# Optimization experiments

Hardware: AMD Instinct MI355X
Metric: run time of the kernel (lower is better)

Reference implementation:

```python
import jax, jax.numpy as jnp
import numpy as np

ETA = 0.15
LAM = 0.05
K = 6


def setup_inputs() -> dict:
    key = jax.random.key(0)
    ks = jax.random.split(key, 9)
    Bsz, L, d, hidden = 32, 8192, 64, 256
    scale = lambda fan_in: 1.0 / np.sqrt(fan_in)
    return {
        "A": jax.random.normal(ks[0], (Bsz, L, d), jnp.float32),
        "B": jax.random.normal(ks[1], (Bsz, L, d), jnp.float32),
        "q": jax.random.normal(ks[2], (Bsz, L, d), jnp.float32),
        "W1": jax.random.normal(ks[3], (2 * d, hidden), jnp.float32) * scale(2 * d),
        "b1": jax.random.normal(ks[4], (hidden,), jnp.float32) * 0.01,
        "W2": jax.random.normal(ks[5], (hidden, d), jnp.float32) * scale(hidden),
        "b2": jax.random.normal(ks[6], (d,), jnp.float32) * 0.01,
        "Wq": jax.random.normal(ks[7], (d, d), jnp.float32) * scale(d),
        "bq": jax.random.normal(ks[8], (d,), jnp.float32) * 0.01,
    }


def _smooth1d(x):
    return x - LAM * (2.0 * x - jnp.roll(x, 1, axis=1) - jnp.roll(x, -1, axis=1))


def reference(A, B, q, W1, b1, W2, b2, Wq, bq):
    # mu_net: Linear -> ReLU -> Linear -> Softplus on concat([A,B])
    h = jnp.concatenate([A, B], axis=-1)  # [B, L, 2d]
    mu = jax.nn.softplus(jax.nn.relu(h @ W1 + b1) @ W2 + b2)  # [B, L, d]
    gate = jnp.tanh(q @ Wq + bq)
    mu = mu * (1.0 + 0.5 * gate)

    hA, hB = A, B
    for _ in range(K):
        step = ETA * (mu * (hA - hB))
        hA = _smooth1d(hA - step)
        hB = _smooth1d(hB + step)

    energy = 0.5 * jnp.sum(mu * jnp.square(hA - hB), axis=(1, 2))  # [B]
    return hA, hB, energy
```

## Files before the change

kernel.cpp:

```cpp
#include <hip/hip_runtime.h>
#include <hip/hip_bf16.h>
#include <hip/hip_fp16.h>

#define ETA 0.15f
#define LAM 0.05f

typedef unsigned int uint32;
typedef __attribute__((ext_vector_type(8))) short short8;
typedef __attribute__((ext_vector_type(4))) float floatx4;

static const int BSZ = 32, LL = 8192, DD = 64;
static const int RTOT = BSZ * LL;

static const size_t MU_BYTES = (size_t)RTOT * DD * 2;
static const size_t W1T_OFF  = MU_BYTES;
static const size_t W2T_OFF  = W1T_OFF + 256 * 128 * 2;
static const size_t WQT_OFF  = W2T_OFF + 64 * 256 * 2;

__device__ __forceinline__ unsigned short f2bf(float f) {
    uint32 u = __builtin_bit_cast(uint32, f);
    uint32 r = (u + 0x7FFFu + ((u >> 16) & 1u)) >> 16;
    return (unsigned short)r;
}

__device__ __forceinline__ float fast_softplus(float x) {
    return fmaxf(x, 0.f) + __logf(1.f + __expf(-fabsf(x)));
}
__device__ __forceinline__ float fast_tanh(float x) {
    float t = __expf(-2.f * fabsf(x));
    float r = (1.f - t) / (1.f + t);
    return copysignf(r, x);
}

__global__ void prep_kernel(const float* __restrict__ W1, const float* __restrict__ W2,
                            const float* __restrict__ Wq,
                            unsigned short* __restrict__ w1t, unsigned short* __restrict__ w2t,
                            unsigned short* __restrict__ wqt, float* __restrict__ energy) {
    int tid = blockIdx.x * blockDim.x + threadIdx.x;
    int nth = gridDim.x * blockDim.x;
    for (int i = tid; i < 256 * 128; i += nth) { int n = i >> 7, k = i & 127; w1t[i] = f2bf(W1[k * 256 + n]); }
    for (int i = tid; i < 64 * 256; i += nth) { int n = i >> 8, k = i & 255; w2t[i] = f2bf(W2[k * 64 + n]); }
    for (int i = tid; i < 64 * 64;  i += nth) { int n = i >> 6, k = i & 63;  wqt[i] = f2bf(Wq[k * 64 + n]); }
    if (tid < 32) energy[tid] = 0.f;
}

__global__ __launch_bounds__(256) void mlp_kernel(
    const float* __restrict__ A, const float* __restrict__ B, const float* __restrict__ Q,
    const float* __restrict__ b1, const float* __restrict__ b2, const float* __restrict__ bq,
    const unsigned short* __restrict__ w1t, const unsigned short* __restrict__ w2t,
    const unsigned short* __restrict__ wqt, _Float16* __restrict__ mu_out) {
    __shared__ char lds[61440];
    unsigned short* Xs = (unsigned short*)(lds);
    unsigned short* Zs = (unsigned short*)(lds + 17408);
    unsigned short* Qs = (unsigned short*)(lds + 17408 + 34816);

    const int tid = threadIdx.x;
    const int lane = tid & 63;
    const int w = tid >> 6;
    const int q4 = lane >> 4;
    const int l16 = lane & 15;
    const int rowbase = blockIdx.x * 64;

    uint32* Xu = (uint32*)Xs;
    for (int i = tid; i < 64 * 64; i += 256) {
        int r = i >> 6, j2 = i & 63;
        const float* src = (j2 < 32) ? (A + (size_t)(rowbase + r) * 64 + 2 * j2)
                                     : (B + (size_t)(rowbase + r) * 64 + 2 * (j2 - 32));
        float2 v = *(const float2*)src;
        Xu[r * 68 + j2] = (uint32)f2bf(v.x) | ((uint32)f2bf(v.y) << 16);
    }
    uint32* Qu = (uint32*)Qs;
    for (int i = tid; i < 64 * 32; i += 256) {
        int r = i >> 5, j2 = i & 31;
        float2 v = *(const float2*)(Q + (size_t)(rowbase + r) * 64 + 2 * j2);
        Qu[r * 36 + j2] = (uint32)f2bf(v.x) | ((uint32)f2bf(v.y) << 16);
    }
    __syncthreads();

    short8 ax[4][4];
#pragma unroll
    for (int m = 0; m < 4; m++)
#pragma unroll
        for (int kt = 0; kt < 4; kt++)
            ax[m][kt] = *(const short8*)&Xs[(m * 16 + l16) * 136 + kt * 32 + q4 * 8];

#pragma unroll
    for (int nt = 0; nt < 4; nt++) {
        const int ng = w * 4 + nt;
        short8 wf[4];
#pragma unroll
        for (int kt = 0; kt < 4; kt++)
            wf[kt] = *(const short8*)&w1t[(ng * 16 + l16) * 128 + kt * 32 + q4 * 8];
        floatx4 acc[4];
#pragma unroll
        for (int m = 0; m < 4; m++) acc[m] = (floatx4){0.f, 0.f, 0.f, 0.f};
#pragma unroll
        for (int kt = 0; kt < 4; kt++)
#pragma unroll
            for (int m = 0; m < 4; m++)
                acc[m] = __builtin_amdgcn_mfma_f32_16x16x32_bf16(ax[m][kt], wf[kt], acc[m], 0, 0, 0);
        const int col = ng * 16 + l16;
        const float b1v = b1[col];
#pragma unroll
        for (int m = 0; m < 4; m++)
#pragma unroll
            for (int r = 0; r < 4; r++) {
                float z = acc[m][r] + b1v;
                z = z > 0.f ? z : 0.f;
                Zs[(m * 16 + q4 * 4 + r) * 272 + col] = f2bf(z);
            }
    }
    short8 w2f[8], wqf[2];
#pragma unroll
    for (int kt = 0; kt < 8; kt++)
        w2f[kt] = *(const short8*)&w2t[(w * 16 + l16) * 256 + kt * 32 + q4 * 8];
#pragma unroll
    for (int kt = 0; kt < 2; kt++)
        wqf[kt] = *(const short8*)&wqt[(w * 16 + l16) * 64 + kt * 32 + q4 * 8];
    __syncthreads();

    floatx4 acc2[4], acc3[4];
#pragma unroll
    for (int m = 0; m < 4; m++) { acc2[m] = (floatx4){0.f,0.f,0.f,0.f}; acc3[m] = (floatx4){0.f,0.f,0.f,0.f}; }
#pragma unroll
    for (int m = 0; m < 4; m++)
#pragma unroll
        for (int kt = 0; kt < 8; kt++) {
            short8 az = *(const short8*)&Zs[(m * 16 + l16) * 272 + kt * 32 + q4 * 8];
            acc2[m] = __builtin_amdgcn_mfma_f32_16x16x32_bf16(az, w2f[kt], acc2[m], 0, 0, 0);
        }
#pragma unroll
    for (int m = 0; m < 4; m++)
#pragma unroll
        for (int kt = 0; kt < 2; kt++) {
            short8 aq = *(const short8*)&Qs[(m * 16 + l16) * 72 + kt * 32 + q4 * 8];
            acc3[m] = __builtin_amdgcn_mfma_f32_16x16x32_bf16(aq, wqf[kt], acc3[m], 0, 0, 0);
        }
    const int col = w * 16 + l16;
    const float b2v = b2[col], bqv = bq[col];
#pragma unroll
    for (int m = 0; m < 4; m++)
#pragma unroll
        for (int r = 0; r < 4; r++) {
            int row = m * 16 + q4 * 4 + r;
            float sp = fast_softplus(acc2[m][r] + b2v);
            float g = fast_tanh(acc3[m][r] + bqv);
            float mu = sp * (1.f + 0.5f * g);
            mu_out[(size_t)(rowbase + row) * 64 + col] = (_Float16)mu;
        }
}

__global__ __launch_bounds__(256) void iter_kernel(
    const float* __restrict__ A, const float* __restrict__ B, const _Float16* __restrict__ mu_ws,
    float* __restrict__ outA, float* __restrict__ outB, float* __restrict__ energy) {
    __shared__ float ex[2][4][4][64];
    __shared__ float esm[4];
    const int tid = threadIdx.x;
    const int col = tid & 63;
    const int g = tid >> 6;
    const int b = blockIdx.y;
    const int s = blockIdx.x * 64;
    const size_t bbase = (size_t)b * 8192;
    const int r0 = g * 19;

    float a[19], bv[19], me[19];
#pragma unroll
    for (int i = 0; i < 19; i++) {
        int gl = (s + r0 + i + 8192 - 6) & 8191;
        size_t idx = (bbase + gl) * 64 + col;
        a[i] = A[idx];
        bv[i] = B[idx];
        me[i] = ETA * (float)mu_ws[idx];
    }
    for (int it = 0; it < 6; it++) {
        float st[19];
#pragma unroll
        for (int i = 0; i < 19; i++) st[i] = me[i] * (a[i] - bv[i]);
        float* exb = &ex[it & 1][0][0][0];
        exb[0 * 256 + g * 64 + col] = a[0] - st[0];
        exb[1 * 256 + g * 64 + col] = a[18] - st[18];
        exb[2 * 256 + g * 64 + col] = bv[0] + st[0];
        exb[3 * 256 + g * 64 + col] = bv[18] + st[18];
        __syncthreads();
        float tAup = (g > 0) ? exb[1 * 256 + (g - 1) * 64 + col] : a[0] - st[0];
        float tAdn = (g < 3) ? exb[0 * 256 + (g + 1) * 64 + col] : a[18] - st[18];
        float tBup = (g > 0) ? exb[3 * 256 + (g - 1) * 64 + col] : bv[0] + st[0];
        float tBdn = (g < 3) ? exb[2 * 256 + (g + 1) * 64 + col] : bv[18] + st[18];
        float prev = tAup, cur = a[0] - st[0];
#pragma unroll
        for (int i = 0; i < 19; i++) {
            float nxt = (i < 18) ? (a[i + 1] - st[i + 1]) : tAdn;
            a[i] = cur - LAM * (2.f * cur - prev - nxt);
            prev = cur; cur = nxt;
        }
        prev = tBup; cur = bv[0] + st[0];
#pragma unroll
        for (int i = 0; i < 19; i++) {
            float nxt = (i < 18) ? (bv[i + 1] + st[i + 1]) : tBdn;
            bv[i] = cur - LAM * (2.f * cur - prev - nxt);
            prev = cur; cur = nxt;
        }
    }
    float e = 0.f;
#pragma unroll
    for (int i = 0; i < 19; i++) {
        int r = r0 + i;
        if (r >= 6 && r < 70) {
            float d = a[i] - bv[i];
            e += me[i] * d * d;
            size_t gidx = (bbase + s + (r - 6)) * 64 + col;
            outA[gidx] = a[i];
            outB[gidx] = bv[i];
        }
    }
    e *= 0.5f / ETA;
#pragma unroll
    for (int off = 32; off > 0; off >>= 1) e += __shfl_down(e, off, 64);
    if ((tid & 63) == 0) esm[g] = e;
    __syncthreads();
    if (tid == 0) atomicAdd(energy + b, esm[0] + esm[1] + esm[2] + esm[3]);
}

extern "C" void kernel_launch(void* const* d_in, const int* in_sizes, int n_in,
                              void* d_out, int out_size, void* d_ws, size_t ws_size,
                              hipStream_t stream) {
    const float* A  = (const float*)d_in[0];
    const float* B  = (const float*)d_in[1];
    const float* Q  = (const float*)d_in[2];
    const float* W1 = (const float*)d_in[3];
    const float* b1 = (const float*)d_in[4];
    const float* W2 = (const float*)d_in[5];
    const float* b2 = (const float*)d_in[6];
    const float* Wq = (const float*)d_in[7];
    const float* bq = (const float*)d_in[8];

    float* outA = (float*)d_out;
    float* outB = outA + (size_t)RTOT * 64;
    float* energy = outB + (size_t)RTOT * 64;

    char* ws = (char*)d_ws;
    _Float16* mu_ws = (_Float16*)ws;
    unsigned short* w1t = (unsigned short*)(ws + W1T_OFF);
    unsigned short* w2t = (unsigned short*)(ws + W2T_OFF);
    unsigned short* wqt = (unsigned short*)(ws + WQT_OFF);

    hipLaunchKernelGGL(prep_kernel, dim3(64), dim3(256), 0, stream,
                       W1, W2, Wq, w1t, w2t, wqt, energy);
    hipLaunchKernelGGL(mlp_kernel, dim3(RTOT / 64), dim3(256), 0, stream,
                       A, B, Q, b1, b2, bq, w1t, w2t, wqt, mu_ws);
    hipLaunchKernelGGL(iter_kernel, dim3(LL / 64, BSZ), dim3(256), 0, stream,
                       A, B, mu_ws, outA, outB, energy);
}
```

Before: 414.1 us.

## Vectorize iter kernel with float4 rows and shrink MLP LDS by aliasing buffers

The iteration kernel now gives each thread 4 adjacent columns as float4 and splits a 80-row window (halo 8) across 16 row groups of 5 rows, replacing 19 scalar rows per thread. This is meant to cut register pressure and use wider global and LDS accesses, at the cost of more halo recomputation per tile. The MLP kernel computes the gate GEMM first and then reuses the X region for Z, shrinking LDS from 60KB to 34KB so more blocks fit per CU. That reuse needs an extra barrier.

```diff
diff --git a/kernel.cpp b/kernel.cpp
--- a/kernel.cpp
+++ b/kernel.cpp
@@ -8,6 +8,7 @@
 typedef unsigned int uint32;
 typedef __attribute__((ext_vector_type(8))) short short8;
 typedef __attribute__((ext_vector_type(4))) float floatx4;
+typedef __attribute__((ext_vector_type(4))) _Float16 half4;
 
 static const int BSZ = 32, LL = 8192, DD = 64;
 static const int RTOT = BSZ * LL;
@@ -22,7 +23,6 @@
     uint32 r = (u + 0x7FFFu + ((u >> 16) & 1u)) >> 16;
     return (unsigned short)r;
 }
-
 __device__ __forceinline__ float fast_softplus(float x) {
     return fmaxf(x, 0.f) + __logf(1.f + __expf(-fabsf(x)));
 }
@@ -49,10 +49,10 @@
     const float* __restrict__ b1, const float* __restrict__ b2, const float* __restrict__ bq,
     const unsigned short* __restrict__ w1t, const unsigned short* __restrict__ w2t,
     const unsigned short* __restrict__ wqt, _Float16* __restrict__ mu_out) {
-    __shared__ char lds[61440];
+    __shared__ char lds[34816];
     unsigned short* Xs = (unsigned short*)(lds);
-    unsigned short* Zs = (unsigned short*)(lds + 17408);
-    unsigned short* Qs = (unsigned short*)(lds + 17408 + 34816);
+    unsigned short* Qs = (unsigned short*)(lds + 17408);
+    unsigned short* Zs = (unsigned short*)(lds);
 
     const int tid = threadIdx.x;
     const int lane = tid & 63;
@@ -77,12 +77,29 @@
     }
     __syncthreads();
 
+    floatx4 acc3[4];
+#pragma unroll
+    for (int m = 0; m < 4; m++) acc3[m] = (floatx4){0.f, 0.f, 0.f, 0.f};
+    {
+        short8 wqf[2];
+#pragma unroll
+        for (int kt = 0; kt < 2; kt++)
+            wqf[kt] = *(const short8*)&wqt[(w * 16 + l16) * 64 + kt * 32 + q4 * 8];
+#pragma unroll
+        for (int m = 0; m < 4; m++)
+#pragma unroll
+            for (int kt = 0; kt < 2; kt++) {
+                short8 aq = *(const short8*)&Qs[(m * 16 + l16) * 72 + kt * 32 + q4 * 8];
+                acc3[m] = __builtin_amdgcn_mfma_f32_16x16x32_bf16(aq, wqf[kt], acc3[m], 0, 0, 0);
+            }
+    }
     short8 ax[4][4];
 #pragma unroll
     for (int m = 0; m < 4; m++)
 #pragma unroll
         for (int kt = 0; kt < 4; kt++)
             ax[m][kt] = *(const short8*)&Xs[(m * 16 + l16) * 136 + kt * 32 + q4 * 8];
+    __syncthreads();
 
 #pragma unroll
     for (int nt = 0; nt < 4; nt++) {
@@ -110,31 +127,21 @@
                 Zs[(m * 16 + q4 * 4 + r) * 272 + col] = f2bf(z);
             }
     }
-    short8 w2f[8], wqf[2];
+    short8 w2f[8];
 #pragma unroll
     for (int kt = 0; kt < 8; kt++)
         w2f[kt] = *(const short8*)&w2t[(w * 16 + l16) * 256 + kt * 32 + q4 * 8];
-#pragma unroll
-    for (int kt = 0; kt < 2; kt++)
-        wqf[kt] = *(const short8*)&wqt[(w * 16 + l16) * 64 + kt * 32 + q4 * 8];
-    __syncthreads();
-
-    floatx4 acc2[4], acc3[4];
-#pragma unroll
-    for (int m = 0; m < 4; m++) { acc2[m] = (floatx4){0.f,0.f,0.f,0.f}; acc3[m] = (floatx4){0.f,0.f,0.f,0.f}; }
+    __syncthreads();
+
+    floatx4 acc2[4];
+#pragma unroll
+    for (int m = 0; m < 4; m++) acc2[m] = (floatx4){0.f, 0.f, 0.f, 0.f};
 #pragma unroll
     for (int m = 0; m < 4; m++)
 #pragma unroll
         for (int kt = 0; kt < 8; kt++) {
             short8 az = *(const short8*)&Zs[(m * 16 + l16) * 272 + kt * 32 + q4 * 8];
             acc2[m] = __builtin_amdgcn_mfma_f32_16x16x32_bf16(az, w2f[kt], acc2[m], 0, 0, 0);
-        }
-#pragma unroll
-    for (int m = 0; m < 4; m++)
-#pragma unroll
-        for (int kt = 0; kt < 2; kt++) {
-            short8 aq = *(const short8*)&Qs[(m * 16 + l16) * 72 + kt * 32 + q4 * 8];
-            acc3[m] = __builtin_amdgcn_mfma_f32_16x16x32_bf16(aq, wqf[kt], acc3[m], 0, 0, 0);
         }
     const int col = w * 16 + l16;
     const float b2v = b2[col], bqv = bq[col];
@@ -153,70 +160,75 @@
 __global__ __launch_bounds__(256) void iter_kernel(
     const float* __restrict__ A, const float* __restrict__ B, const _Float16* __restrict__ mu_ws,
     float* __restrict__ outA, float* __restrict__ outB, float* __restrict__ energy) {
-    __shared__ float ex[2][4][4][64];
+    __shared__ float ex[2][4][16][64];
     __shared__ float esm[4];
     const int tid = threadIdx.x;
-    const int col = tid & 63;
-    const int g = tid >> 6;
+    const int c4 = tid & 15;
+    const int g = tid >> 4;
     const int b = blockIdx.y;
     const int s = blockIdx.x * 64;
     const size_t bbase = (size_t)b * 8192;
-    const int r0 = g * 19;
-
-    float a[19], bv[19], me[19];
-#pragma unroll
-    for (int i = 0; i < 19; i++) {
-        int gl = (s + r0 + i + 8192 - 6) & 8191;
-        size_t idx = (bbase + gl) * 64 + col;
-        a[i] = A[idx];
-        bv[i] = B[idx];
-        me[i] = ETA * (float)mu_ws[idx];
+    const int r0 = g * 5;
+
+    floatx4 a[5], bv[5], me[5];
+#pragma unroll
+    for (int i = 0; i < 5; i++) {
+        int gl = (s + r0 + i + 8192 - 8) & 8191;
+        size_t base = (bbase + gl) * 64 + c4 * 4;
+        a[i] = *(const floatx4*)(A + base);
+        bv[i] = *(const floatx4*)(B + base);
+        half4 m4 = *(const half4*)(mu_ws + base);
+        me[i] = __builtin_convertvector(m4, floatx4) * ETA;
     }
     for (int it = 0; it < 6; it++) {
-        float st[19];
-#pragma unroll
-        for (int i = 0; i < 19; i++) st[i] = me[i] * (a[i] - bv[i]);
-        float* exb = &ex[it & 1][0][0][0];
-        exb[0 * 256 + g * 64 + col] = a[0] - st[0];
-        exb[1 * 256 + g * 64 + col] = a[18] - st[18];
-        exb[2 * 256 + g * 64 + col] = bv[0] + st[0];
-        exb[3 * 256 + g * 64 + col] = bv[18] + st[18];
+#pragma unroll
+        for (int i = 0; i < 5; i++) {
+            floatx4 st = me[i] * (a[i] - bv[i]);
+            a[i] = a[i] - st;
+            bv[i] = bv[i] + st;
+        }
+        const int p = it & 1;
+        *(floatx4*)&ex[p][0][g][c4 * 4] = a[0];
+        *(floatx4*)&ex[p][1][g][c4 * 4] = a[4];
+        *(floatx4*)&ex[p][2][g][c4 * 4] = bv[0];
+        *(floatx4*)&ex[p][3][g][c4 * 4] = bv[4];
         __syncthreads();
-        float tAup = (g > 0) ? exb[1 * 256 + (g - 1) * 64 + col] : a[0] - st[0];
-        float tAdn = (g < 3) ? exb[0 * 256 + (g + 1) * 64 + col] : a[18] - st[18];
-        float tBup = (g > 0) ? exb[3 * 256 + (g - 1) * 64 + col] : bv[0] + st[0];
-        float tBdn = (g < 3) ? exb[2 * 256 + (g + 1) * 64 + col] : bv[18] + st[18];
-        float prev = tAup, cur = a[0] - st[0];
-#pragma unroll
-        for (int i = 0; i < 19; i++) {
-            float nxt = (i < 18) ? (a[i + 1] - st[i + 1]) : tAdn;
+        floatx4 aUp = (g > 0)  ? *(const floatx4*)&ex[p][1][g - 1][c4 * 4] : a[0];
+        floatx4 aDn = (g < 15) ? *(const floatx4*)&ex[p][0][g + 1][c4 * 4] : a[4];
+        floatx4 bUp = (g > 0)  ? *(const floatx4*)&ex[p][3][g - 1][c4 * 4] : bv[0];
+        floatx4 bDn = (g < 15) ? *(const floatx4*)&ex[p][2][g + 1][c4 * 4] : bv[4];
+        floatx4 prev = aUp, cur = a[0];
+#pragma unroll
+        for (int i = 0; i < 5; i++) {
+            floatx4 nxt = (i < 4) ? a[i + 1] : aDn;
             a[i] = cur - LAM * (2.f * cur - prev - nxt);
             prev = cur; cur = nxt;
         }
-        prev = tBup; cur = bv[0] + st[0];
-#pragma unroll
-        for (int i = 0; i < 19; i++) {
-            float nxt = (i < 18) ? (bv[i + 1] + st[i + 1]) : tBdn;
+        prev = bUp; cur = bv[0];
+#pragma unroll
+        for (int i = 0; i < 5; i++) {
+            floatx4 nxt = (i < 4) ? bv[i + 1] : bDn;
             bv[i] = cur - LAM * (2.f * cur - prev - nxt);
             prev = cur; cur = nxt;
         }
     }
     float e = 0.f;
 #pragma unroll
-    for (int i = 0; i < 19; i++) {
-        int r = r0 + i;
-        if (r >= 6 && r < 70) {
-            float d = a[i] - bv[i];
-            e += me[i] * d * d;
-            size_t gidx = (bbase + s + (r - 6)) * 64 + col;
-            outA[gidx] = a[i];
-            outB[gidx] = bv[i];
+    for (int i = 0; i < 5; i++) {
+        int wr = r0 + i;
+        if (wr >= 8 && wr < 72) {
+            floatx4 d = a[i] - bv[i];
+            floatx4 q = me[i] * d * d;
+            e += q.x + q.y + q.z + q.w;
+            size_t gidx = (bbase + s + (wr - 8)) * 64 + c4 * 4;
+            *(floatx4*)(outA + gidx) = a[i];
+            *(floatx4*)(outB + gidx) = bv[i];
         }
     }
     e *= 0.5f / ETA;
 #pragma unroll
     for (int off = 32; off > 0; off >>= 1) e += __shfl_down(e, off, 64);
-    if ((tid & 63) == 0) esm[g] = e;
+    if ((tid & 63) == 0) esm[tid >> 6] = e;
     __syncthreads();
     if (tid == 0) atomicAdd(energy + b, esm[0] + esm[1] + esm[2] + esm[3]);
 }
```

Result: no change. 409.8 us (-1.0%).
